# Performance work log

Measured on AMD Instinct MI355X. Metric: run time of the kernel, lower is better.

Reference implementation:

```python
import jax, jax.numpy as jnp
import numpy as np

B, H, O, DEPTH = 1024, 256, 32, 6  # batch, hidden(=latent), symbol vocab, full-binary-tree depth


def _lin(x, w, b):
    return x @ w.T + b


def _gru(x, h, wx, wh, bx, bh):
    # GRUAncestral / GRUFraternal cell: r,z,n gates, out = (1-z)*n + z*h
    r = jax.nn.sigmoid(_lin(x, wx[0], bx[0]) + _lin(h, wh[0], bh[0]))
    z = jax.nn.sigmoid(_lin(x, wx[1], bx[1]) + _lin(h, wh[1], bh[1]))
    n = jnp.tanh(_lin(x, wx[2], bx[2]) + r * _lin(h, wh[2], bh[2]))
    return (1.0 - z) * n + z * h


def setup_inputs() -> dict:
    key = jax.random.key(0)
    ks = jax.random.split(key, 16)
    def w(k, shape):
        fan_in = shape[-1]
        return jax.random.normal(k, shape, jnp.float32) * (1.0 / np.sqrt(fan_in))
    return {
        "z": jax.random.normal(ks[0], (B, 1, H), jnp.float32),
        "h2o_w": w(ks[1], (O, H)), "h2o_b": jnp.zeros((O,), jnp.float32),
        "w_c_w": w(ks[2], (H, H)), "w_c_b": jnp.zeros((H,), jnp.float32),
        "w_d_w": w(ks[3], (H, H)), "w_d_b": jnp.zeros((H,), jnp.float32),
        "z2h1_w": w(ks[4], (H, H)), "z2h1_b": jnp.zeros((H,), jnp.float32),
        "z2h2_w": w(ks[5], (H, H)), "z2h2_b": jnp.zeros((H,), jnp.float32),
        "gru_a_wx": w(ks[6], (3, H, O)), "gru_a_wh": w(ks[7], (3, H, H)),
        "gru_a_bx": jnp.zeros((3, H), jnp.float32), "gru_a_bh": jnp.zeros((3, H), jnp.float32),
        "gru_s_wx": w(ks[8], (3, H, O)), "gru_s_wh": w(ks[9], (3, H, H)),
        "gru_s_bx": jnp.zeros((3, H), jnp.float32), "gru_s_bh": jnp.zeros((3, H), jnp.float32),
        "depth": DEPTH,
    }


def reference(z, h2o_w, h2o_b, w_c_w, w_c_b, w_d_w, w_d_b,
              z2h1_w, z2h1_b, z2h2_w, z2h2_b,
              gru_a_wx, gru_a_wh, gru_a_bx, gru_a_bh,
              gru_s_wx, gru_s_wh, gru_s_bx, gru_s_bh,
              depth):
    preds = []  # preorder list of per-node predictions

    def rec(hidden_a, hidden, d):
        pred = _lin(hidden, h2o_w, h2o_b)          # [B,1,O]
        preds.append(pred)
        sp = jax.nn.softmax(pred, axis=2)
        if d > 1:
            # first child
            hf, spf = rec(_lin(hidden_a, w_c_w, w_c_b), _lin(hidden, w_d_w, w_d_b), d - 1)
            # second child: fraternal update on sibling state + ancestral update
            hf = _gru(spf, hf, gru_s_wx, gru_s_wh, gru_s_bx, gru_s_bh)
            hidden2 = hf + _gru(sp, hidden_a, gru_a_wx, gru_a_wh, gru_a_bx, gru_a_bh)
            rec(_lin(hidden_a, w_c_w, w_c_b), _lin(hidden2, w_d_w, w_d_b), d - 1)
        return hidden, sp

    rec(_lin(z, z2h1_w, z2h1_b), _lin(z, z2h2_w, z2h2_b), int(depth))
    return jnp.stack(preds)  # [2**depth-1, B, 1, O]
```

## Files before the change

kernel.cpp:

```cpp
#include <hip/hip_runtime.h>
#include <math.h>

#define Bdim 1024
#define DEPTHC 6

typedef __attribute__((ext_vector_type(8))) _Float16 f16x8;
typedef __attribute__((ext_vector_type(4))) float f32x4;

__device__ __forceinline__ unsigned short f2h(float x) {
    _Float16 h = (_Float16)x;
    unsigned short u;
    __builtin_memcpy(&u, &h, 2);
    return u;
}
__device__ __forceinline__ float h2f(unsigned short u) {
    _Float16 h;
    __builtin_memcpy(&h, &u, 2);
    return (float)h;
}
__device__ __forceinline__ float sigmf(float x) { return 1.0f / (1.0f + expf(-x)); }

__device__ __forceinline__ void glds16(const void* g, void* l) {
    __builtin_amdgcn_global_load_lds(
        (const __attribute__((address_space(1))) unsigned int*)g,
        (__attribute__((address_space(3))) unsigned int*)l, 16, 0, 0);
}

__device__ __forceinline__ void sbar() { asm volatile("s_barrier" ::: "memory"); }
template<int N> __device__ __forceinline__ void vmwait() {
    static_assert(N == 0 || N == 6 || N == 8 || N == 10, "unsupported vmcnt");
    if constexpr (N == 0)  asm volatile("s_waitcnt vmcnt(0)" ::: "memory");
    if constexpr (N == 6)  asm volatile("s_waitcnt vmcnt(6)" ::: "memory");
    if constexpr (N == 8)  asm volatile("s_waitcnt vmcnt(8)" ::: "memory");
    if constexpr (N == 10) asm volatile("s_waitcnt vmcnt(10)" ::: "memory");
    __builtin_amdgcn_sched_barrier(0);
}

__device__ __forceinline__ int preorder_idx(int level, int q) {
    int idx = 0, rem = DEPTHC;
    for (int k = level - 1; k >= 0; --k) {
        int b = (q >> k) & 1;
        idx += 1 + b * ((1 << (rem - 1)) - 1);
        rem--;
    }
    return idx;
}

struct CvtEnt { const float* src; unsigned short* dst; int n; int klog2; int pad; };
struct CvtArgs { CvtEnt e[8]; };

__global__ __launch_bounds__(256) void cvt_f16(CvtArgs a) {
    CvtEnt E = a.e[blockIdx.y];
    const int k = 1 << E.klog2;
    for (int t = blockIdx.x * 256 + threadIdx.x; t < E.n; t += gridDim.x * 256) {
        const float x = E.src[t];
        const int r = t >> E.klog2, c = t & (k - 1);
        if (!E.pad) {
            E.dst[(size_t)r * k + c] = f2h(x);
        } else {
            E.dst[(size_t)r * 2 * k + c] = f2h(x);
            E.dst[(size_t)r * 2 * k + k + c] = 0;
        }
    }
}

template<int BM>
__global__ __launch_bounds__(256) void mfma_gemm(
    const unsigned short* __restrict__ A2, const unsigned short* __restrict__ W2,
    const float* __restrict__ bias, float* __restrict__ Cf, int Nf,
    unsigned short* __restrict__ C2, int outStride, int outOffset)
{
    constexpr int MF = BM / 32;
    constexpr int AI = BM / 32;
    __shared__ __attribute__((aligned(16))) unsigned short As[2][BM * 64];
    __shared__ __attribute__((aligned(16))) unsigned short Ws[2][8192];

    const int tid = threadIdx.x;
    const int w = tid >> 6, lane = tid & 63;
    const int m0 = blockIdx.x * BM, col0 = blockIdx.y * 128;
    const int p = m0 >> 10;
    const int wm = (w >> 1) * (BM / 2), wn = (w & 1) << 6;

    f32x4 acc[MF][4] = {};

    auto stage = [&](int buf, int s) {
        const int ka = s << 6;
        #pragma unroll
        for (int i = 0; i < AI; ++i) {
            const int r = w * (BM / 4) + (i << 3) + (lane >> 3);
            const int sl = (lane & 7) ^ (r & 7);
            glds16(A2 + (size_t)(m0 + r) * 256 + ka + (sl << 3),
                   &As[buf][(w * (BM / 4) + (i << 3)) << 6]);
        }
        #pragma unroll
        for (int i = 0; i < 4; ++i) {
            const int r = (w << 5) + (i << 3) + (lane >> 3);
            const int sl = (lane & 7) ^ (r & 7);
            glds16(W2 + (size_t)(col0 + r) * 256 + ka + (sl << 3),
                   &Ws[buf][(w << 11) + (i << 9)]);
        }
    };
    auto compute = [&](int buf) {
        #pragma unroll
        for (int kk = 0; kk < 2; ++kk) {
            f16x8 af[MF], bw[4];
            #pragma unroll
            for (int mf = 0; mf < MF; ++mf) {
                const int row = wm + (mf << 4) + (lane & 15);
                const int sl = (((kk << 2) | (lane >> 4)) ^ (row & 7)) << 3;
                af[mf] = *(const f16x8*)&As[buf][(row << 6) + sl];
            }
            #pragma unroll
            for (int nf = 0; nf < 4; ++nf) {
                const int row = wn + (nf << 4) + (lane & 15);
                const int sl = (((kk << 2) | (lane >> 4)) ^ (row & 7)) << 3;
                bw[nf] = *(const f16x8*)&Ws[buf][(row << 6) + sl];
            }
            __builtin_amdgcn_s_setprio(1);
            #pragma unroll
            for (int mf = 0; mf < MF; ++mf)
                #pragma unroll
                for (int nf = 0; nf < 4; ++nf)
                    acc[mf][nf] = __builtin_amdgcn_mfma_f32_16x16x32_f16(
                        af[mf], bw[nf], acc[mf][nf], 0, 0, 0);
            __builtin_amdgcn_s_setprio(0);
        }
    };

    stage(0, 0);
    #pragma unroll
    for (int s = 0; s < 4; ++s) {
        if (s + 1 < 4) { stage((s + 1) & 1, s + 1); vmwait<AI + 4>(); }
        else           { vmwait<0>(); }
        sbar();
        compute(s & 1);
        sbar();
    }

    const size_t oBase = (((size_t)(p * outStride + outOffset)) << 10) + (m0 & 1023);
    #pragma unroll
    for (int nf = 0; nf < 4; ++nf) {
        const int col = col0 + wn + (nf << 4) + (lane & 15);
        const float bj = bias[col];
        #pragma unroll
        for (int mf = 0; mf < MF; ++mf) {
            const int rb = wm + (mf << 4) + ((lane >> 4) << 2);
            #pragma unroll
            for (int r = 0; r < 4; ++r) {
                const float v = acc[mf][nf][r] + bj;
                const size_t orow = oBase + rb + r;
                if (Cf) Cf[orow * (size_t)Nf + col] = v;
                if (C2) C2[orow * 256 + col] = f2h(v);
            }
        }
    }
}

__global__ __launch_bounds__(256) void pred_softmax(
    const unsigned short* __restrict__ H2, const float* __restrict__ h2o_w,
    const float* __restrict__ h2o_b, float* __restrict__ out,
    unsigned short* __restrict__ SP2, int level, int nodeStride, int nodeOffset)
{
    __shared__ float wsm[32][260];
    __shared__ float hsm[8][260];

    const int tid = threadIdx.x;
    const int p   = blockIdx.x >> 7;
    const int b0  = (blockIdx.x & 127) * 8;
    const int q   = p * nodeStride + nodeOffset;
    const unsigned short* Hrow = H2 + ((size_t)q * Bdim + b0) * 256;

    for (int t = tid * 4; t < 32 * 256; t += 1024) {
        const float4 v = *(const float4*)(h2o_w + t);
        const int j = t >> 8, k = t & 255;
        wsm[j][k] = v.x; wsm[j][k + 1] = v.y; wsm[j][k + 2] = v.z; wsm[j][k + 3] = v.w;
    }
    for (int t = tid * 4; t < 8 * 256; t += 1024) {
        const int r = t >> 8, k = t & 255;
        const ushort4 v4 = *(const ushort4*)(Hrow + (size_t)r * 256 + k);
        hsm[r][k + 0] = h2f(v4.x);
        hsm[r][k + 1] = h2f(v4.y);
        hsm[r][k + 2] = h2f(v4.z);
        hsm[r][k + 3] = h2f(v4.w);
    }
    __syncthreads();

    const int r = tid >> 5;
    const int j = tid & 31;
    float acc = 0.f;
    #pragma unroll 4
    for (int k = 0; k < 256; k += 4) {
        const float4 hv = *(const float4*)&hsm[r][k];
        const float4 wv = *(const float4*)&wsm[j][k];
        acc = fmaf(hv.x, wv.x, acc);
        acc = fmaf(hv.y, wv.y, acc);
        acc = fmaf(hv.z, wv.z, acc);
        acc = fmaf(hv.w, wv.w, acc);
    }
    acc += h2o_b[j];

    const int idx = preorder_idx(level, q);
    const int b   = b0 + r;
    out[((size_t)idx * Bdim + b) * 32 + j] = acc;

    float mx = acc;
    #pragma unroll
    for (int off = 16; off > 0; off >>= 1) mx = fmaxf(mx, __shfl_xor(mx, off, 32));
    const float e = expf(acc - mx);
    float sum = e;
    #pragma unroll
    for (int off = 16; off > 0; off >>= 1) sum += __shfl_xor(sum, off, 32);
    const float sp = e / sum;

    const size_t sbase = ((size_t)q * Bdim + b) * 64;
    SP2[sbase + j] = f2h(sp);
    SP2[sbase + 32 + j] = 0;
}

__global__ __launch_bounds__(256) void gru_a_kernel(
    const unsigned short* __restrict__ SP2c, const float* __restrict__ GhA,
    const float* __restrict__ wx, const float* __restrict__ bx,
    const float* __restrict__ ha, unsigned short* __restrict__ Apart)
{
    __shared__ float sps[16][33];
    const int tid = threadIdx.x;
    const int m0  = blockIdx.x * 16;

    for (int t = tid; t < 16 * 32; t += 256) {
        const int r = t >> 5, k = t & 31;
        sps[r][k] = h2f(SP2c[((size_t)(m0 + r)) * 64 + k]);
    }
    __syncthreads();

    const int j = tid;
    float accr[16] = {}, accz[16] = {}, accn[16] = {};
    const float* wxj = wx + (size_t)j * 32;
    for (int k = 0; k < 32; ++k) {
        const float wr_ = wxj[k];
        const float wz_ = wxj[8192 + k];
        const float wn_ = wxj[16384 + k];
        #pragma unroll
        for (int r = 0; r < 16; ++r) {
            const float s = sps[r][k];
            accr[r] = fmaf(s, wr_, accr[r]);
            accz[r] = fmaf(s, wz_, accz[r]);
            accn[r] = fmaf(s, wn_, accn[r]);
        }
    }
    const float bxr = bx[j], bxz = bx[256 + j], bxn = bx[512 + j];
    #pragma unroll
    for (int r = 0; r < 16; ++r) {
        const int m = m0 + r;
        const int b = m & 1023;
        const float ghr = GhA[(size_t)b * 768 + j];
        const float ghz = GhA[(size_t)b * 768 + 256 + j];
        const float ghn = GhA[(size_t)b * 768 + 512 + j];
        const float rg = sigmf(accr[r] + bxr + ghr);
        const float zg = sigmf(accz[r] + bxz + ghz);
        const float ng = tanhf(accn[r] + bxn + rg * ghn);
        Apart[(size_t)m * 256 + j] = f2h((1.f - zg) * ng + zg * ha[(size_t)b * 256 + j]);
    }
}

template<int BM>
__global__ __launch_bounds__(256) void gru_s_fused(
    const unsigned short* __restrict__ Hn2, const unsigned short* __restrict__ SP2n,
    const unsigned short* __restrict__ gsW2, const unsigned short* __restrict__ gsX2,
    const float* __restrict__ gs_bx, const float* __restrict__ gs_bh,
    const unsigned short* __restrict__ Apf, unsigned short* __restrict__ Ap2)
{
    constexpr int MF = BM / 32;
    constexpr int AI = BM / 32;
    __shared__ __attribute__((aligned(16))) unsigned short As[2][BM * 64];
    __shared__ __attribute__((aligned(16))) unsigned short Ws[2][12288];

    const int tid = threadIdx.x;
    const int w = tid >> 6, lane = tid & 63;
    const int col0 = blockIdx.y * 64;
    const int m0 = blockIdx.x * BM;
    const int p = m0 >> 10;
    const size_t aBase = (((size_t)(2 * p)) << 10) + (m0 & 1023);
    const int wr = w >> 1, wc = w & 1;

    f32x4 a_sr[MF][2] = {}, a_sz[MF][2] = {}, a_snh[MF][2] = {}, a_snx[MF][2] = {};

    auto stage = [&](int buf, int s) {
        #pragma unroll
        for (int i = 0; i < AI; ++i) {
            const int r = w * (BM / 4) + (i << 3) + (lane >> 3);
            const int sl = (lane & 7) ^ (r & 7);
            const unsigned short* src;
            if (s < 4) src = Hn2 + (aBase + r) * 256 + (s << 6) + (sl << 3);
            else       src = SP2n + (aBase + r) * 64 + (sl << 3);
            glds16(src, &As[buf][(w * (BM / 4) + (i << 3)) << 6]);
        }
        #pragma unroll
        for (int j = 0; j < 6; ++j) {
            const int R = w * 48 + (j << 3) + (lane >> 3);
            const int g = R >> 6, c = R & 63;
            const int sl = (lane & 7) ^ (R & 7);
            const size_t grow = (size_t)(g * 256 + col0 + c);
            const unsigned short* src;
            if (s < 4) src = gsW2 + grow * 256 + (s << 6) + (sl << 3);
            else       src = gsX2 + grow * 64 + (sl << 3);
            glds16(src, &Ws[buf][(w * 48 + (j << 3)) << 6]);
        }
    };

    auto compute = [&](int buf, f32x4 (*tr)[2], f32x4 (*tz)[2], f32x4 (*tn)[2]) {
        #pragma unroll
        for (int kk = 0; kk < 2; ++kk) {
            f16x8 af[MF], bw[3][2];
            #pragma unroll
            for (int mf = 0; mf < MF; ++mf) {
                const int row = wr * (BM / 2) + (mf << 4) + (lane & 15);
                const int sl = (((kk << 2) | (lane >> 4)) ^ (row & 7)) << 3;
                af[mf] = *(const f16x8*)&As[buf][(row << 6) + sl];
            }
            #pragma unroll
            for (int g = 0; g < 3; ++g)
                #pragma unroll
                for (int nf = 0; nf < 2; ++nf) {
                    const int R = (g << 6) + (wc << 5) + (nf << 4) + (lane & 15);
                    const int sl = (((kk << 2) | (lane >> 4)) ^ (R & 7)) << 3;
                    bw[g][nf] = *(const f16x8*)&Ws[buf][(R << 6) + sl];
                }
            __builtin_amdgcn_s_setprio(1);
            #pragma unroll
            for (int mf = 0; mf < MF; ++mf)
                #pragma unroll
                for (int nf = 0; nf < 2; ++nf) {
                    tr[mf][nf] = __builtin_amdgcn_mfma_f32_16x16x32_f16(af[mf], bw[0][nf], tr[mf][nf], 0, 0, 0);
                    tz[mf][nf] = __builtin_amdgcn_mfma_f32_16x16x32_f16(af[mf], bw[1][nf], tz[mf][nf], 0, 0, 0);
                    tn[mf][nf] = __builtin_amdgcn_mfma_f32_16x16x32_f16(af[mf], bw[2][nf], tn[mf][nf], 0, 0, 0);
                }
            __builtin_amdgcn_s_setprio(0);
        }
    };

    stage(0, 0);
    #pragma unroll
    for (int s = 0; s < 5; ++s) {
        if (s + 1 < 5) { stage((s + 1) & 1, s + 1); vmwait<AI + 6>(); }
        else           { vmwait<0>(); }
        sbar();
        if (s < 4) compute(s & 1, a_sr, a_sz, a_snh);
        else       compute(s & 1, a_sr, a_sz, a_snx);
        sbar();
    }

    #pragma unroll
    for (int nf = 0; nf < 2; ++nf) {
        const int jc = col0 + (wc << 5) + (nf << 4) + (lane & 15);
        const float bsr  = gs_bx[jc] + gs_bh[jc];
        const float bsz  = gs_bx[256 + jc] + gs_bh[256 + jc];
        const float bsnx = gs_bx[512 + jc];
        const float bsnh = gs_bh[512 + jc];
        #pragma unroll
        for (int mf = 0; mf < MF; ++mf) {
            #pragma unroll
            for (int r = 0; r < 4; ++r) {
                const int rowl = wr * (BM / 2) + (mf << 4) + ((lane >> 4) << 2) + r;
                const int m = m0 + rowl;
                const float rs = sigmf(a_sr[mf][nf][r] + bsr);
                const float zs = sigmf(a_sz[mf][nf][r] + bsz);
                const float ns = tanhf(a_snx[mf][nf][r] + bsnx + rs * (a_snh[mf][nf][r] + bsnh));
                const float hv = h2f(Hn2[(aBase + rowl) * 256 + jc]);
                const float val = (1.f - zs) * ns + zs * hv + h2f(Apf[(size_t)m * 256 + jc]);
                Ap2[(size_t)m * 256 + jc] = f2h(val);
            }
        }
    }
}

extern "C" void kernel_launch(void* const* d_in, const int* in_sizes, int n_in,
                              void* d_out, int out_size, void* d_ws, size_t ws_size,
                              hipStream_t stream) {
    (void)in_sizes; (void)n_in; (void)out_size;

    const float* z      = (const float*)d_in[0];
    const float* h2o_w  = (const float*)d_in[1];
    const float* h2o_b  = (const float*)d_in[2];
    const float* w_c_w  = (const float*)d_in[3];
    const float* w_c_b  = (const float*)d_in[4];
    const float* w_d_w  = (const float*)d_in[5];
    const float* w_d_b  = (const float*)d_in[6];
    const float* z2h1_w = (const float*)d_in[7];
    const float* z2h1_b = (const float*)d_in[8];
    const float* z2h2_w = (const float*)d_in[9];
    const float* z2h2_b = (const float*)d_in[10];
    const float* ga_wx  = (const float*)d_in[11];
    const float* ga_wh  = (const float*)d_in[12];
    const float* ga_bx  = (const float*)d_in[13];
    const float* ga_bh  = (const float*)d_in[14];
    const float* gs_wx  = (const float*)d_in[15];
    const float* gs_wh  = (const float*)d_in[16];
    const float* gs_bx  = (const float*)d_in[17];
    const float* gs_bh  = (const float*)d_in[18];

    float* out = (float*)d_out;

    size_t off = 0;
    auto alloc = [&](size_t bytes) -> void* {
        void* r = (char*)d_ws + off;
        off += (bytes + 255) & ~(size_t)255;
        return r;
    };
    unsigned short* H2a  = (unsigned short*)alloc(16ull * 1024 * 256 * 2);
    unsigned short* H2b  = (unsigned short*)alloc(32ull * 1024 * 256 * 2);
    unsigned short* SP2a = (unsigned short*)alloc(16ull * 1024 * 64 * 2);
    unsigned short* SP2b = (unsigned short*)alloc(32ull * 1024 * 64 * 2);
    float* hacF0 = (float*)alloc(1024ull * 256 * 4);
    float* hacF1 = (float*)alloc(1024ull * 256 * 4);
    unsigned short* hac20 = (unsigned short*)alloc(1024ull * 256 * 2);
    unsigned short* hac21 = (unsigned short*)alloc(1024ull * 256 * 2);
    float* GhA = (float*)alloc(1024ull * 768 * 4);
    unsigned short* Apf = (unsigned short*)alloc(16ull * 1024 * 256 * 2);
    unsigned short* Ap2 = (unsigned short*)alloc(16ull * 1024 * 256 * 2);
    unsigned short* z2  = (unsigned short*)alloc(1024ull * 256 * 2);
    unsigned short* wd2 = (unsigned short*)alloc(256ull * 256 * 2);
    unsigned short* wc2 = (unsigned short*)alloc(256ull * 256 * 2);
    unsigned short* z12 = (unsigned short*)alloc(256ull * 256 * 2);
    unsigned short* z22 = (unsigned short*)alloc(256ull * 256 * 2);
    unsigned short* gaW2 = (unsigned short*)alloc(768ull * 256 * 2);
    unsigned short* gsW2 = (unsigned short*)alloc(768ull * 256 * 2);
    unsigned short* gsX2 = (unsigned short*)alloc(768ull * 64 * 2);
    if (off > ws_size) return;

    const dim3 blk(256);

    CvtArgs ca = {{
        { z,      z2,   1024 * 256, 8, 0 },
        { w_d_w,  wd2,  256 * 256,  8, 0 },
        { w_c_w,  wc2,  256 * 256,  8, 0 },
        { z2h1_w, z12,  256 * 256,  8, 0 },
        { z2h2_w, z22,  256 * 256,  8, 0 },
        { ga_wh,  gaW2, 768 * 256,  8, 0 },
        { gs_wh,  gsW2, 768 * 256,  8, 0 },
        { gs_wx,  gsX2, 768 * 32,   5, 1 },
    }};
    cvt_f16<<<dim3(64, 8), blk, 0, stream>>>(ca);

    mfma_gemm<64><<<dim3(16, 2), blk, 0, stream>>>(z2, z12, z2h1_b, hacF0, 256, hac20, 1, 0);
    mfma_gemm<64><<<dim3(16, 2), blk, 0, stream>>>(z2, z22, z2h2_b, nullptr, 0, H2a, 1, 0);
    pred_softmax<<<dim3(128), blk, 0, stream>>>(H2a, h2o_w, h2o_b, out, SP2a, 0, 1, 0);

    unsigned short* cur2 = H2a;  unsigned short* nxt2 = H2b;
    unsigned short* spc  = SP2a; unsigned short* spn  = SP2b;
    float* hf = hacF0;  float* hn = hacF1;
    unsigned short* hf2 = hac20; unsigned short* hn2 = hac21;

    for (int l = 0; l < DEPTHC - 1; ++l) {
        const int M = (1 << l) * Bdim;
        const bool small = (M <= 8192);

        if (small) mfma_gemm<64><<<dim3(M / 64, 2), blk, 0, stream>>>(cur2, wd2, w_d_b, nullptr, 0, nxt2, 2, 0);
        else       mfma_gemm<128><<<dim3(M / 128, 2), blk, 0, stream>>>(cur2, wd2, w_d_b, nullptr, 0, nxt2, 2, 0);
        pred_softmax<<<dim3(M / 8), blk, 0, stream>>>(nxt2, h2o_w, h2o_b, out, spn, l + 1, 2, 0);
        mfma_gemm<64><<<dim3(16, 6), blk, 0, stream>>>(hf2, gaW2, ga_bh, GhA, 768, nullptr, 1, 0);
        gru_a_kernel<<<dim3(M / 16), blk, 0, stream>>>(spc, GhA, ga_wx, ga_bx, hf, Apf);
        if (small) gru_s_fused<64><<<dim3(M / 64, 4), blk, 0, stream>>>(nxt2, spn, gsW2, gsX2, gs_bx, gs_bh, Apf, Ap2);
        else       gru_s_fused<128><<<dim3(M / 128, 4), blk, 0, stream>>>(nxt2, spn, gsW2, gsX2, gs_bx, gs_bh, Apf, Ap2);
        if (small) mfma_gemm<64><<<dim3(M / 64, 2), blk, 0, stream>>>(Ap2, wd2, w_d_b, nullptr, 0, nxt2, 2, 1);
        else       mfma_gemm<128><<<dim3(M / 128, 2), blk, 0, stream>>>(Ap2, wd2, w_d_b, nullptr, 0, nxt2, 2, 1);
        pred_softmax<<<dim3(M / 8), blk, 0, stream>>>(nxt2, h2o_w, h2o_b, out, spn, l + 1, 2, 1);
        mfma_gemm<64><<<dim3(16, 2), blk, 0, stream>>>(hf2, wc2, w_c_b, hn, 256, hn2, 1, 0);

        unsigned short* t2;
        t2 = cur2; cur2 = nxt2; nxt2 = t2;
        t2 = spc;  spc  = spn;  spn  = t2;
        float* tf = hf; hf = hn; hn = tf;
        t2 = hf2; hf2 = hn2; hn2 = t2;
    }
}
```

Measured before the change: 495.0 us.

## Batch independent GEMMs into grouped launches and fuse pred with GRU-ancestral

Merges the independent GEMMs of each level (w_d child GEMM, GRU-ancestral hidden GEMM, w_c GEMM) into one grouped launch, and also merges the initial two z GEMMs. The pred/softmax kernel and the GRU-ancestral elementwise kernel now share one launch. The Apf intermediate is written in a fragment-tiled layout so gru_s_fused can read it with vector loads, and the hidden value is taken from shared memory instead of global. The aim is fewer launches, better occupancy on small levels and less global traffic, at the cost of block-index dispatch branches and a larger shared-memory footprint in the merged kernel. The last level skips the unused w_c GEMM.

```diff
diff --git a/kernel.cpp b/kernel.cpp
--- a/kernel.cpp
+++ b/kernel.cpp
@@ -65,19 +65,19 @@
 }
 
 template<int BM>
-__global__ __launch_bounds__(256) void mfma_gemm(
+__device__ __forceinline__ void gemm_body(
+    int m0, int col0,
     const unsigned short* __restrict__ A2, const unsigned short* __restrict__ W2,
     const float* __restrict__ bias, float* __restrict__ Cf, int Nf,
-    unsigned short* __restrict__ C2, int outStride, int outOffset)
+    unsigned short* __restrict__ C2, int outStride, int outOffset,
+    unsigned short* As, unsigned short* Ws)
 {
     constexpr int MF = BM / 32;
     constexpr int AI = BM / 32;
-    __shared__ __attribute__((aligned(16))) unsigned short As[2][BM * 64];
-    __shared__ __attribute__((aligned(16))) unsigned short Ws[2][8192];
+    constexpr int ASZ = BM * 64;
 
     const int tid = threadIdx.x;
     const int w = tid >> 6, lane = tid & 63;
-    const int m0 = blockIdx.x * BM, col0 = blockIdx.y * 128;
     const int p = m0 >> 10;
     const int wm = (w >> 1) * (BM / 2), wn = (w & 1) << 6;
 
@@ -90,14 +90,14 @@
             const int r = w * (BM / 4) + (i << 3) + (lane >> 3);
             const int sl = (lane & 7) ^ (r & 7);
             glds16(A2 + (size_t)(m0 + r) * 256 + ka + (sl << 3),
-                   &As[buf][(w * (BM / 4) + (i << 3)) << 6]);
+                   &As[buf * ASZ + ((w * (BM / 4) + (i << 3)) << 6)]);
         }
         #pragma unroll
         for (int i = 0; i < 4; ++i) {
             const int r = (w << 5) + (i << 3) + (lane >> 3);
             const int sl = (lane & 7) ^ (r & 7);
             glds16(W2 + (size_t)(col0 + r) * 256 + ka + (sl << 3),
-                   &Ws[buf][(w << 11) + (i << 9)]);
+                   &Ws[buf * 8192 + (w << 11) + (i << 9)]);
         }
     };
     auto compute = [&](int buf) {
@@ -108,13 +108,13 @@
             for (int mf = 0; mf < MF; ++mf) {
                 const int row = wm + (mf << 4) + (lane & 15);
                 const int sl = (((kk << 2) | (lane >> 4)) ^ (row & 7)) << 3;
-                af[mf] = *(const f16x8*)&As[buf][(row << 6) + sl];
+                af[mf] = *(const f16x8*)&As[buf * ASZ + (row << 6) + sl];
             }
             #pragma unroll
             for (int nf = 0; nf < 4; ++nf) {
                 const int row = wn + (nf << 4) + (lane & 15);
                 const int sl = (((kk << 2) | (lane >> 4)) ^ (row & 7)) << 3;
-                bw[nf] = *(const f16x8*)&Ws[buf][(row << 6) + sl];
+                bw[nf] = *(const f16x8*)&Ws[buf * 8192 + (row << 6) + sl];
             }
             __builtin_amdgcn_s_setprio(1);
             #pragma unroll
@@ -156,109 +156,155 @@
     }
 }
 
-__global__ __launch_bounds__(256) void pred_softmax(
+template<int BM>
+__global__ __launch_bounds__(256) void mfma_gemm(
+    const unsigned short* __restrict__ A2, const unsigned short* __restrict__ W2,
+    const float* __restrict__ bias, float* __restrict__ Cf, int Nf,
+    unsigned short* __restrict__ C2, int outStride, int outOffset)
+{
+    __shared__ __attribute__((aligned(16))) unsigned short As[2 * BM * 64];
+    __shared__ __attribute__((aligned(16))) unsigned short Ws[2 * 8192];
+    gemm_body<BM>(blockIdx.x * BM, blockIdx.y * 128, A2, W2, bias, Cf, Nf, C2,
+                  outStride, outOffset, As, Ws);
+}
+
+struct GDesc {
+    const unsigned short* A; const unsigned short* W; const float* bias;
+    float* Cf; int Nf; unsigned short* C2; int outStride; int outOffset; int nbm;
+};
+struct GMulti { GDesc d[3]; int n0; int n01; };
+
+template<int BM>
+__global__ __launch_bounds__(256) void mfma_gemm_multi(GMulti g) {
+    __shared__ __attribute__((aligned(16))) unsigned short As[2 * BM * 64];
+    __shared__ __attribute__((aligned(16))) unsigned short Ws[2 * 8192];
+    const int id = blockIdx.x;
+    int di, base;
+    if (id < g.n0)       { di = 0; base = 0; }
+    else if (id < g.n01) { di = 1; base = g.n0; }
+    else                 { di = 2; base = g.n01; }
+    const GDesc D = g.d[di];
+    const int lid = id - base;
+    gemm_body<BM>((lid % D.nbm) * BM, (lid / D.nbm) * 128, D.A, D.W, D.bias,
+                  D.Cf, D.Nf, D.C2, D.outStride, D.outOffset, As, Ws);
+}
+
+__global__ __launch_bounds__(256) void pred_grua(
     const unsigned short* __restrict__ H2, const float* __restrict__ h2o_w,
     const float* __restrict__ h2o_b, float* __restrict__ out,
-    unsigned short* __restrict__ SP2, int level, int nodeStride, int nodeOffset)
+    unsigned short* __restrict__ SP2, int level, int nodeStride, int nodeOffset,
+    int npred,
+    const unsigned short* __restrict__ SP2c, const float* __restrict__ GhA,
+    const float* __restrict__ wx, const float* __restrict__ bx,
+    const float* __restrict__ ha, unsigned short* __restrict__ ApfP)
 {
     __shared__ float wsm[32][260];
     __shared__ float hsm[8][260];
 
     const int tid = threadIdx.x;
-    const int p   = blockIdx.x >> 7;
-    const int b0  = (blockIdx.x & 127) * 8;
-    const int q   = p * nodeStride + nodeOffset;
-    const unsigned short* Hrow = H2 + ((size_t)q * Bdim + b0) * 256;
-
-    for (int t = tid * 4; t < 32 * 256; t += 1024) {
-        const float4 v = *(const float4*)(h2o_w + t);
-        const int j = t >> 8, k = t & 255;
-        wsm[j][k] = v.x; wsm[j][k + 1] = v.y; wsm[j][k + 2] = v.z; wsm[j][k + 3] = v.w;
-    }
-    for (int t = tid * 4; t < 8 * 256; t += 1024) {
-        const int r = t >> 8, k = t & 255;
-        const ushort4 v4 = *(const ushort4*)(Hrow + (size_t)r * 256 + k);
-        hsm[r][k + 0] = h2f(v4.x);
-        hsm[r][k + 1] = h2f(v4.y);
-        hsm[r][k + 2] = h2f(v4.z);
-        hsm[r][k + 3] = h2f(v4.w);
-    }
-    __syncthreads();
-
-    const int r = tid >> 5;
-    const int j = tid & 31;
-    float acc = 0.f;
-    #pragma unroll 4
-    for (int k = 0; k < 256; k += 4) {
-        const float4 hv = *(const float4*)&hsm[r][k];
-        const float4 wv = *(const float4*)&wsm[j][k];
-        acc = fmaf(hv.x, wv.x, acc);
-        acc = fmaf(hv.y, wv.y, acc);
-        acc = fmaf(hv.z, wv.z, acc);
-        acc = fmaf(hv.w, wv.w, acc);
-    }
-    acc += h2o_b[j];
-
-    const int idx = preorder_idx(level, q);
-    const int b   = b0 + r;
-    out[((size_t)idx * Bdim + b) * 32 + j] = acc;
-
-    float mx = acc;
-    #pragma unroll
-    for (int off = 16; off > 0; off >>= 1) mx = fmaxf(mx, __shfl_xor(mx, off, 32));
-    const float e = expf(acc - mx);
-    float sum = e;
-    #pragma unroll
-    for (int off = 16; off > 0; off >>= 1) sum += __shfl_xor(sum, off, 32);
-    const float sp = e / sum;
-
-    const size_t sbase = ((size_t)q * Bdim + b) * 64;
-    SP2[sbase + j] = f2h(sp);
-    SP2[sbase + 32 + j] = 0;
-}
-
-__global__ __launch_bounds__(256) void gru_a_kernel(
-    const unsigned short* __restrict__ SP2c, const float* __restrict__ GhA,
-    const float* __restrict__ wx, const float* __restrict__ bx,
-    const float* __restrict__ ha, unsigned short* __restrict__ Apart)
-{
-    __shared__ float sps[16][33];
-    const int tid = threadIdx.x;
-    const int m0  = blockIdx.x * 16;
-
-    for (int t = tid; t < 16 * 32; t += 256) {
-        const int r = t >> 5, k = t & 31;
-        sps[r][k] = h2f(SP2c[((size_t)(m0 + r)) * 64 + k]);
-    }
-    __syncthreads();
-
-    const int j = tid;
-    float accr[16] = {}, accz[16] = {}, accn[16] = {};
-    const float* wxj = wx + (size_t)j * 32;
-    for (int k = 0; k < 32; ++k) {
-        const float wr_ = wxj[k];
-        const float wz_ = wxj[8192 + k];
-        const float wn_ = wxj[16384 + k];
+
+    if ((int)blockIdx.x < npred) {
+        const int bid = blockIdx.x;
+        const int p   = bid >> 7;
+        const int b0  = (bid & 127) * 8;
+        const int q   = p * nodeStride + nodeOffset;
+        const unsigned short* Hrow = H2 + ((size_t)q * Bdim + b0) * 256;
+
+        for (int t = tid * 4; t < 32 * 256; t += 1024) {
+            const float4 v = *(const float4*)(h2o_w + t);
+            const int j = t >> 8, k = t & 255;
+            wsm[j][k] = v.x; wsm[j][k + 1] = v.y; wsm[j][k + 2] = v.z; wsm[j][k + 3] = v.w;
+        }
+        for (int t = tid * 4; t < 8 * 256; t += 1024) {
+            const int r = t >> 8, k = t & 255;
+            const ushort4 v4 = *(const ushort4*)(Hrow + (size_t)r * 256 + k);
+            hsm[r][k + 0] = h2f(v4.x);
+            hsm[r][k + 1] = h2f(v4.y);
+            hsm[r][k + 2] = h2f(v4.z);
+            hsm[r][k + 3] = h2f(v4.w);
+        }
+        __syncthreads();
+
+        const int r = tid >> 5;
+        const int j = tid & 31;
+        float acc = 0.f;
+        #pragma unroll 4
+        for (int k = 0; k < 256; k += 4) {
+            const float4 hv = *(const float4*)&hsm[r][k];
+            const float4 wv = *(const float4*)&wsm[j][k];
+            acc = fmaf(hv.x, wv.x, acc);
+            acc = fmaf(hv.y, wv.y, acc);
+            acc = fmaf(hv.z, wv.z, acc);
+            acc = fmaf(hv.w, wv.w, acc);
+        }
+        acc += h2o_b[j];
+
+        const int idx = preorder_idx(level, q);
+        const int b   = b0 + r;
+        out[((size_t)idx * Bdim + b) * 32 + j] = acc;
+
+        float mx = acc;
+        #pragma unroll
+        for (int off = 16; off > 0; off >>= 1) mx = fmaxf(mx, __shfl_xor(mx, off, 32));
+        const float e = expf(acc - mx);
+        float sum = e;
+        #pragma unroll
+        for (int off = 16; off > 0; off >>= 1) sum += __shfl_xor(sum, off, 32);
+        const float sp = e / sum;
+
+        const size_t sbase = ((size_t)q * Bdim + b) * 64;
+        SP2[sbase + j] = f2h(sp);
+        SP2[sbase + 32 + j] = 0;
+    } else {
+        float (*sps)[33] = (float(*)[33])hsm;
+        const int bid = blockIdx.x - npred;
+        const int m0  = bid * 16;
+
+        for (int t = tid; t < 16 * 32; t += 256) {
+            const int r = t >> 5, k = t & 31;
+            sps[r][k] = h2f(SP2c[((size_t)(m0 + r)) * 64 + k]);
+        }
+        __syncthreads();
+
+        const int j = tid;
+        float accr[16] = {}, accz[16] = {}, accn[16] = {};
+        const float* wxj = wx + (size_t)j * 32;
+        for (int k = 0; k < 32; ++k) {
+            const float wr_ = wxj[k];
+            const float wz_ = wxj[8192 + k];
+            const float wn_ = wxj[16384 + k];
+            #pragma unroll
+            for (int r = 0; r < 16; ++r) {
+                const float s = sps[r][k];
+                accr[r] = fmaf(s, wr_, accr[r]);
+                accz[r] = fmaf(s, wz_, accz[r]);
+                accn[r] = fmaf(s, wn_, accn[r]);
+            }
+        }
+        const float bxr = bx[j], bxz = bx[256 + j], bxn = bx[512 + j];
+        float vals[16];
         #pragma unroll
         for (int r = 0; r < 16; ++r) {
-            const float s = sps[r][k];
-            accr[r] = fmaf(s, wr_, accr[r]);
-            accz[r] = fmaf(s, wz_, accz[r]);
-            accn[r] = fmaf(s, wn_, accn[r]);
-        }
-    }
-    const float bxr = bx[j], bxz = bx[256 + j], bxn = bx[512 + j];
-    #pragma unroll
-    for (int r = 0; r < 16; ++r) {
-        const int m = m0 + r;
-        const int b = m & 1023;
-        const float ghr = GhA[(size_t)b * 768 + j];
-        const float ghz = GhA[(size_t)b * 768 + 256 + j];
-        const float ghn = GhA[(size_t)b * 768 + 512 + j];
-        const float rg = sigmf(accr[r] + bxr + ghr);
-        const float zg = sigmf(accz[r] + bxz + ghz);
-        const float ng = tanhf(accn[r] + bxn + rg * ghn);
-        Apart[(size_t)m * 256 + j] = f2h((1.f - zg) * ng + zg * ha[(size_t)b * 256 + j]);
+            const int m = m0 + r;
+            const int b = m & 1023;
+            const float ghr = GhA[(size_t)b * 768 + j];
+            const float ghz = GhA[(size_t)b * 768 + 256 + j];
+            const float ghn = GhA[(size_t)b * 768 + 512 + j];
+            const float rg = sigmf(accr[r] + bxr + ghr);
+            const float zg = sigmf(accz[r] + bxz + ghz);
+            const float ng = tanhf(accn[r] + bxn + rg * ghn);
+            vals[r] = (1.f - zg) * ng + zg * ha[(size_t)b * 256 + j];
+        }
+        const size_t fb = ((size_t)(m0 >> 4) * 16 + (j >> 4)) * 256;
+        #pragma unroll
+        for (int g = 0; g < 4; ++g) {
+            ushort4 st;
+            st.x = f2h(vals[4 * g + 0]);
+            st.y = f2h(vals[4 * g + 1]);
+            st.z = f2h(vals[4 * g + 2]);
+            st.w = f2h(vals[4 * g + 3]);
+            *(ushort4*)(ApfP + fb + ((size_t)((j & 15) + (g << 4)) << 2)) = st;
+        }
     }
 }
 
@@ -267,12 +313,13 @@
     const unsigned short* __restrict__ Hn2, const unsigned short* __restrict__ SP2n,
     const unsigned short* __restrict__ gsW2, const unsigned short* __restrict__ gsX2,
     const float* __restrict__ gs_bx, const float* __restrict__ gs_bh,
-    const unsigned short* __restrict__ Apf, unsigned short* __restrict__ Ap2)
+    const unsigned short* __restrict__ ApfP, unsigned short* __restrict__ Ap2)
 {
     constexpr int MF = BM / 32;
     constexpr int AI = BM / 32;
-    __shared__ __attribute__((aligned(16))) unsigned short As[2][BM * 64];
-    __shared__ __attribute__((aligned(16))) unsigned short Ws[2][12288];
+    constexpr int ASZ = BM * 64;
+    __shared__ __attribute__((aligned(16))) unsigned short As[2 * ASZ];
+    __shared__ __attribute__((aligned(16))) unsigned short Ws[2 * 12288];
 
     const int tid = threadIdx.x;
     const int w = tid >> 6, lane = tid & 63;
@@ -281,8 +328,10 @@
     const int p = m0 >> 10;
     const size_t aBase = (((size_t)(2 * p)) << 10) + (m0 & 1023);
     const int wr = w >> 1, wc = w & 1;
+    const int sc = col0 >> 6;
 
     f32x4 a_sr[MF][2] = {}, a_sz[MF][2] = {}, a_snh[MF][2] = {}, a_snx[MF][2] = {};
+    unsigned short hvv[MF][2][4];
 
     auto stage = [&](int buf, int s) {
         #pragma unroll
@@ -292,7 +341,7 @@
             const unsigned short* src;
             if (s < 4) src = Hn2 + (aBase + r) * 256 + (s << 6) + (sl << 3);
             else       src = SP2n + (aBase + r) * 64 + (sl << 3);
-            glds16(src, &As[buf][(w * (BM / 4) + (i << 3)) << 6]);
+            glds16(src, &As[buf * ASZ + ((w * (BM / 4) + (i << 3)) << 6)]);
         }
         #pragma unroll
         for (int j = 0; j < 6; ++j) {
@@ -303,11 +352,24 @@
             const unsigned short* src;
             if (s < 4) src = gsW2 + grow * 256 + (s << 6) + (sl << 3);
             else       src = gsX2 + grow * 64 + (sl << 3);
-            glds16(src, &Ws[buf][(w * 48 + (j << 3)) << 6]);
+            glds16(src, &Ws[buf * 12288 + ((w * 48 + (j << 3)) << 6)]);
         }
     };
 
-    auto compute = [&](int buf, f32x4 (*tr)[2], f32x4 (*tz)[2], f32x4 (*tn)[2]) {
+    auto compute = [&](int buf, bool dohv, f32x4 (*tr)[2], f32x4 (*tz)[2], f32x4 (*tn)[2]) {
+        if (dohv) {
+            #pragma unroll
+            for (int mf = 0; mf < MF; ++mf)
+                #pragma unroll
+                for (int nf = 0; nf < 2; ++nf)
+                    #pragma unroll
+                    for (int r = 0; r < 4; ++r) {
+                        const int row = wr * (BM / 2) + (mf << 4) + ((lane >> 4) << 2) + r;
+                        const int jcl = (wc << 5) + (nf << 4) + (lane & 15);
+                        hvv[mf][nf][r] =
+                            As[buf * ASZ + (row << 6) + (((jcl >> 3) ^ (row & 7)) << 3) + (jcl & 7)];
+                    }
+        }
         #pragma unroll
         for (int kk = 0; kk < 2; ++kk) {
             f16x8 af[MF], bw[3][2];
@@ -315,7 +377,7 @@
             for (int mf = 0; mf < MF; ++mf) {
                 const int row = wr * (BM / 2) + (mf << 4) + (lane & 15);
                 const int sl = (((kk << 2) | (lane >> 4)) ^ (row & 7)) << 3;
-                af[mf] = *(const f16x8*)&As[buf][(row << 6) + sl];
+                af[mf] = *(const f16x8*)&As[buf * ASZ + (row << 6) + sl];
             }
             #pragma unroll
             for (int g = 0; g < 3; ++g)
@@ -323,7 +385,7 @@
                 for (int nf = 0; nf < 2; ++nf) {
                     const int R = (g << 6) + (wc << 5) + (nf << 4) + (lane & 15);
                     const int sl = (((kk << 2) | (lane >> 4)) ^ (R & 7)) << 3;
-                    bw[g][nf] = *(const f16x8*)&Ws[buf][(R << 6) + sl];
+                    bw[g][nf] = *(const f16x8*)&Ws[buf * 12288 + (R << 6) + sl];
                 }
             __builtin_amdgcn_s_setprio(1);
             #pragma unroll
@@ -344,20 +406,24 @@
         if (s + 1 < 5) { stage((s + 1) & 1, s + 1); vmwait<AI + 6>(); }
         else           { vmwait<0>(); }
         sbar();
-        if (s < 4) compute(s & 1, a_sr, a_sz, a_snh);
-        else       compute(s & 1, a_sr, a_sz, a_snx);
+        if (s < 4) compute(s & 1, s == sc, a_sr, a_sz, a_snh);
+        else       compute(s & 1, false, a_sr, a_sz, a_snx);
         sbar();
     }
 
     #pragma unroll
     for (int nf = 0; nf < 2; ++nf) {
         const int jc = col0 + (wc << 5) + (nf << 4) + (lane & 15);
+        const int jt = (col0 >> 4) + (wc << 1) + nf;
         const float bsr  = gs_bx[jc] + gs_bh[jc];
         const float bsz  = gs_bx[256 + jc] + gs_bh[256 + jc];
         const float bsnx = gs_bx[512 + jc];
         const float bsnh = gs_bh[512 + jc];
         #pragma unroll
         for (int mf = 0; mf < MF; ++mf) {
+            const int gmt = (m0 >> 4) + wr * (BM / 32) + mf;
+            const ushort4 av = *(const ushort4*)(ApfP + ((size_t)gmt * 16 + jt) * 256 + (lane << 2));
+            const unsigned short apv[4] = {av.x, av.y, av.z, av.w};
             #pragma unroll
             for (int r = 0; r < 4; ++r) {
                 const int rowl = wr * (BM / 2) + (mf << 4) + ((lane >> 4) << 2) + r;
@@ -365,8 +431,8 @@
                 const float rs = sigmf(a_sr[mf][nf][r] + bsr);
                 const float zs = sigmf(a_sz[mf][nf][r] + bsz);
                 const float ns = tanhf(a_snx[mf][nf][r] + bsnx + rs * (a_snh[mf][nf][r] + bsnh));
-                const float hv = h2f(Hn2[(aBase + rowl) * 256 + jc]);
-                const float val = (1.f - zs) * ns + zs * hv + h2f(Apf[(size_t)m * 256 + jc]);
+                const float hv = h2f(hvv[mf][nf][r]);
+                const float val = (1.f - zs) * ns + zs * hv + h2f(apv[r]);
                 Ap2[(size_t)m * 256 + jc] = f2h(val);
             }
         }
@@ -415,7 +481,7 @@
     unsigned short* hac20 = (unsigned short*)alloc(1024ull * 256 * 2);
     unsigned short* hac21 = (unsigned short*)alloc(1024ull * 256 * 2);
     float* GhA = (float*)alloc(1024ull * 768 * 4);
-    unsigned short* Apf = (unsigned short*)alloc(16ull * 1024 * 256 * 2);
+    unsigned short* ApfP = (unsigned short*)alloc(16ull * 1024 * 256 * 2);
     unsigned short* Ap2 = (unsigned short*)alloc(16ull * 1024 * 256 * 2);
     unsigned short* z2  = (unsigned short*)alloc(1024ull * 256 * 2);
     unsigned short* wd2 = (unsigned short*)alloc(256ull * 256 * 2);
@@ -441,9 +507,17 @@
     }};
     cvt_f16<<<dim3(64, 8), blk, 0, stream>>>(ca);
 
-    mfma_gemm<64><<<dim3(16, 2), blk, 0, stream>>>(z2, z12, z2h1_b, hacF0, 256, hac20, 1, 0);
-    mfma_gemm<64><<<dim3(16, 2), blk, 0, stream>>>(z2, z22, z2h2_b, nullptr, 0, H2a, 1, 0);
-    pred_softmax<<<dim3(128), blk, 0, stream>>>(H2a, h2o_w, h2o_b, out, SP2a, 0, 1, 0);
+    {
+        GMulti gi;
+        gi.d[0] = { z2, z12, z2h1_b, hacF0, 256, hac20, 1, 0, 16 };
+        gi.d[1] = { z2, z22, z2h2_b, nullptr, 0, H2a, 1, 0, 16 };
+        gi.d[2] = gi.d[1];
+        gi.n0 = 32; gi.n01 = 64;
+        mfma_gemm_multi<64><<<dim3(64), blk, 0, stream>>>(gi);
+    }
+    pred_grua<<<dim3(128), blk, 0, stream>>>(H2a, h2o_w, h2o_b, out, SP2a, 0, 1, 0,
+                                             128, nullptr, nullptr, nullptr, nullptr,
+                                             nullptr, nullptr);
 
     unsigned short* cur2 = H2a;  unsigned short* nxt2 = H2b;
     unsigned short* spc  = SP2a; unsigned short* spn  = SP2b;
@@ -453,18 +527,32 @@
     for (int l = 0; l < DEPTHC - 1; ++l) {
         const int M = (1 << l) * Bdim;
         const bool small = (M <= 8192);
-
-        if (small) mfma_gemm<64><<<dim3(M / 64, 2), blk, 0, stream>>>(cur2, wd2, w_d_b, nullptr, 0, nxt2, 2, 0);
-        else       mfma_gemm<128><<<dim3(M / 128, 2), blk, 0, stream>>>(cur2, wd2, w_d_b, nullptr, 0, nxt2, 2, 0);
-        pred_softmax<<<dim3(M / 8), blk, 0, stream>>>(nxt2, h2o_w, h2o_b, out, spn, l + 1, 2, 0);
-        mfma_gemm<64><<<dim3(16, 6), blk, 0, stream>>>(hf2, gaW2, ga_bh, GhA, 768, nullptr, 1, 0);
-        gru_a_kernel<<<dim3(M / 16), blk, 0, stream>>>(spc, GhA, ga_wx, ga_bx, hf, Apf);
-        if (small) gru_s_fused<64><<<dim3(M / 64, 4), blk, 0, stream>>>(nxt2, spn, gsW2, gsX2, gs_bx, gs_bh, Apf, Ap2);
-        else       gru_s_fused<128><<<dim3(M / 128, 4), blk, 0, stream>>>(nxt2, spn, gsW2, gsX2, gs_bx, gs_bh, Apf, Ap2);
+        const int BMv = small ? 64 : 128;
+        const int nbm = M / BMv;
+        const int nbh = 1024 / BMv;
+
+        {
+            GMulti g1;
+            g1.d[0] = { cur2, wd2, w_d_b, nullptr, 0, nxt2, 2, 0, nbm };
+            g1.d[1] = { hf2, gaW2, ga_bh, GhA, 768, nullptr, 1, 0, nbh };
+            g1.d[2] = { hf2, wc2, w_c_b, hn, 256, hn2, 1, 0, nbh };
+            const int nb0 = nbm * 2, nb1 = nbh * 6;
+            const int nb2 = (l < DEPTHC - 2) ? nbh * 2 : 0;
+            g1.n0 = nb0; g1.n01 = nb0 + nb1;
+            const int ntot = nb0 + nb1 + nb2;
+            if (small) mfma_gemm_multi<64><<<dim3(ntot), blk, 0, stream>>>(g1);
+            else       mfma_gemm_multi<128><<<dim3(ntot), blk, 0, stream>>>(g1);
+        }
+        pred_grua<<<dim3(M / 8 + M / 16), blk, 0, stream>>>(
+            nxt2, h2o_w, h2o_b, out, spn, l + 1, 2, 0, M / 8,
+            spc, GhA, ga_wx, ga_bx, hf, ApfP);
+        if (small) gru_s_fused<64><<<dim3(M / 64, 4), blk, 0, stream>>>(nxt2, spn, gsW2, gsX2, gs_bx, gs_bh, ApfP, Ap2);
+        else       gru_s_fused<128><<<dim3(M / 128, 4), blk, 0, stream>>>(nxt2, spn, gsW2, gsX2, gs_bx, gs_bh, ApfP, Ap2);
         if (small) mfma_gemm<64><<<dim3(M / 64, 2), blk, 0, stream>>>(Ap2, wd2, w_d_b, nullptr, 0, nxt2, 2, 1);
         else       mfma_gemm<128><<<dim3(M / 128, 2), blk, 0, stream>>>(Ap2, wd2, w_d_b, nullptr, 0, nxt2, 2, 1);
-        pred_softmax<<<dim3(M / 8), blk, 0, stream>>>(nxt2, h2o_w, h2o_b, out, spn, l + 1, 2, 1);
-        mfma_gemm<64><<<dim3(16, 2), blk, 0, stream>>>(hf2, wc2, w_c_b, hn, 256, hn2, 1, 0);
+        pred_grua<<<dim3(M / 8), blk, 0, stream>>>(
+            nxt2, h2o_w, h2o_b, out, spn, l + 1, 2, 1, M / 8,
+            nullptr, nullptr, nullptr, nullptr, nullptr, nullptr);
 
         unsigned short* t2;
         t2 = cur2; cur2 = nxt2; nxt2 = t2;
```

Measured after the change: 491.9 us. About the same (-0.6%).
